# Optimization experiments

Measured on AMD Instinct MI355X. Metric: run time of the kernel, lower is better.

The kernel has to match this reference:

```python
import jax, jax.numpy as jnp
import numpy as np

N_NODES = 50000
N_EDGES = 800000
F_IN = 2
T = 12
HID = 64
OUT = 12
K = 2  # diffusion order: identity + 1-hop (out- and in-directed)


def setup_inputs() -> dict:
    key = jax.random.key(0)
    ks = jax.random.split(key, 12)
    inp = {}
    inp["x"] = jax.random.normal(ks[0], (1, N_NODES, F_IN, T), dtype=jnp.float32)
    inp["edge_index"] = jax.random.randint(ks[1], (2, N_EDGES), 0, N_NODES)
    inp["edge_weight"] = jax.random.uniform(ks[2], (N_EDGES,), dtype=jnp.float32)

    def u(k, shape, fan):
        s = 1.0 / np.sqrt(fan)
        return jax.random.uniform(k, shape, jnp.float32, -s, s)

    c1 = F_IN + HID   # 66: DCRNN gates operate on cat([X, H])
    c2 = HID + HID    # 128
    inp["w1z"] = u(ks[3], (2, K, c1, HID), c1); inp["b1z"] = jnp.zeros((HID,), jnp.float32)
    inp["w1r"] = u(ks[4], (2, K, c1, HID), c1); inp["b1r"] = jnp.zeros((HID,), jnp.float32)
    inp["w1h"] = u(ks[5], (2, K, c1, HID), c1); inp["b1h"] = jnp.zeros((HID,), jnp.float32)
    inp["w2z"] = u(ks[6], (2, K, c2, HID), c2); inp["b2z"] = jnp.zeros((HID,), jnp.float32)
    inp["w2r"] = u(ks[7], (2, K, c2, HID), c2); inp["b2r"] = jnp.zeros((HID,), jnp.float32)
    inp["w2h"] = u(ks[8], (2, K, c2, HID), c2); inp["b2h"] = jnp.zeros((HID,), jnp.float32)
    inp["lin_w"] = u(ks[9], (HID, OUT), HID)
    inp["lin_b"] = u(ks[10], (OUT,), HID)
    return inp


def _dconv(X, row, col, norm_out, norm_in, w, b):
    # K=2 diffusion conv: H = X@W[:,0] + (D_O^-1 W diffusion)@W[0,1] + (D_I^-1 W^T diffusion)@W[1,1] + b
    H = X @ w[0, 0] + X @ w[1, 0]
    Xr = X[row]  # gather source-node features per edge: [E, C]
    Tx_o = jax.ops.segment_sum(norm_out[:, None] * Xr, col, num_segments=N_NODES)
    Tx_i = jax.ops.segment_sum(norm_in[:, None] * Xr, col, num_segments=N_NODES)
    return H + Tx_o @ w[0, 1] + Tx_i @ w[1, 1] + b


def _cell(X, H, row, col, no, ni, wz, bz, wr, br, wh, bh):
    # GRU-style DCRNN cell
    XH = jnp.concatenate([X, H], axis=1)
    Z = jax.nn.sigmoid(_dconv(XH, row, col, no, ni, wz, bz))
    R = jax.nn.sigmoid(_dconv(XH, row, col, no, ni, wr, br))
    Ht = jnp.tanh(_dconv(jnp.concatenate([X, R * H], axis=1), row, col, no, ni, wh, bh))
    return Z * H + (1.0 - Z) * Ht


def reference(x, edge_index, edge_weight, w1z, b1z, w1r, b1r, w1h, b1h,
              w2z, b2z, w2r, b2r, w2h, b2h, lin_w, lin_b):
    row, col = edge_index[0], edge_index[1]
    deg_out = jax.ops.segment_sum(edge_weight, row, num_segments=N_NODES)
    deg_in = jax.ops.segment_sum(edge_weight, col, num_segments=N_NODES)
    norm_out = edge_weight / deg_out[row]  # per-edge weight of D_O^{-1} W
    norm_in = edge_weight / deg_in[col]    # per-edge weight of D_I^{-1} W^T
    xs = jnp.transpose(x[0], (2, 0, 1))    # [T, N, F] (batch = 1)

    def step(carry, xt):
        h1, h2 = carry
        h1 = jax.nn.relu(_cell(xt, h1, row, col, norm_out, norm_in, w1z, b1z, w1r, b1r, w1h, b1h))
        h2 = jax.nn.relu(_cell(h1, h2, row, col, norm_out, norm_in, w2z, b2z, w2r, b2r, w2h, b2h))
        return (h1, h2), None

    h0 = jnp.zeros((N_NODES, HID), x.dtype)
    (h1, h2), _ = jax.lax.scan(step, (h0, h0), xs)
    out = h2 @ lin_w + lin_b  # [N, 12]
    return out.reshape(1, N_NODES, OUT)
```

## Files before the change

### kernel.cpp

```cpp
#include <hip/hip_runtime.h>

#define NN 50000
#define NE 800000
#define TT 12
#define NBIN (4 * NN)
#define NBLK ((NBIN + 255) / 256)

typedef _Float16 h16;
typedef __attribute__((ext_vector_type(2))) _Float16 h16x2;
typedef __attribute__((ext_vector_type(4))) _Float16 h16x4;
typedef __attribute__((ext_vector_type(8))) _Float16 half8;
typedef __attribute__((ext_vector_type(4))) float f32x4;
typedef __attribute__((address_space(3))) h16 as3h16;
typedef __attribute__((address_space(3))) half8 as3half8;

static constexpr size_t alignup(size_t x) { return (x + 255) & ~(size_t)255; }
static constexpr size_t O_CNT  = 0;
static constexpr size_t O_CUR  = alignup(O_CNT + NBIN + 1);
static constexpr size_t O_DEGO = alignup(O_CUR + NBIN);
static constexpr size_t O_BSUM = alignup(O_DEGO + NN);
static constexpr size_t O_BEXC = O_BSUM + 1024;
static constexpr size_t O_EDG  = alignup(O_BEXC + 1024);
static constexpr size_t O_TXX  = alignup(O_EDG + (size_t)NE * 2);
static constexpr size_t O_WF1ZR= alignup(O_TXX + (size_t)TT * NN * 4);
static constexpr size_t O_WF1H = alignup(O_WF1ZR + 12288);
static constexpr size_t O_WF2ZR= alignup(O_WF1H + 6144);
static constexpr size_t O_WF2H = alignup(O_WF2ZR + 24576);
static constexpr size_t O_WX1ZR= alignup(O_WF2H + 12288);
static constexpr size_t O_WX1H = alignup(O_WX1ZR + 768);
static constexpr size_t O_PX0  = alignup(O_WX1H + 384);
static constexpr size_t O_PX1  = O_PX0 + (size_t)NN * 64;
static constexpr size_t O_PZR  = O_PX1 + (size_t)NN * 64;
static constexpr size_t O_Z1   = O_PZR + (size_t)NN * 64;
static constexpr size_t O_Z2   = O_Z1 + (size_t)NN * 32;
static constexpr size_t O_TXA  = alignup(O_Z2 + (size_t)NN * 32);
static constexpr size_t O_TXB  = alignup(O_TXA + (size_t)NN * 64);
static constexpr size_t WS_FLOATS = O_TXB + (size_t)NN * 128;

__device__ __forceinline__ float sigm_(float x) { return 1.f / (1.f + __expf(-x)); }
__device__ __forceinline__ float tanh_(float x) { float e = __expf(2.f * x); return 1.f - 2.f / (e + 1.f); }

__device__ __forceinline__ void gld_lds16(const h16* g, as3h16* l) {
    __builtin_amdgcn_global_load_lds(
        (const __attribute__((address_space(1))) void*)g,
        (__attribute__((address_space(3))) void*)l, 16, 0, 0);
}


__global__ __launch_bounds__(256) void k_zero(float* ws) {
    size_t i = (size_t)blockIdx.x * 256 + threadIdx.x;
    size_t stride = (size_t)gridDim.x * 256;
    for (size_t p = i; p < O_BSUM + 2048; p += stride) ((int*)ws)[p] = 0;
    for (size_t p = i; p < (size_t)NN * 128; p += stride) ws[O_PX0 + p] = 0.f;
    for (size_t p = i; p < (size_t)NN * 128; p += stride) ws[O_TXB + p] = 0.f;
}

__global__ __launch_bounds__(256) void k_hist(const int* ei, float* ws) {
    int e = blockIdx.x * 256 + threadIdx.x;
    if (e >= NE) return;
    int r = ei[e], c = ei[NE + e];
    int bin = c * 4 + r / 12500;
    int rk = atomicAdd((int*)ws + O_CNT + bin, 1);
    ((int*)ws)[O_TXX + e] = rk;
}

__global__ __launch_bounds__(256) void k_scanA(float* ws) {
    __shared__ int sh[256];
    int t = threadIdx.x, i = blockIdx.x * 256 + t;
    int v = (i < NBIN) ? ((int*)ws)[O_CNT + i] : 0;
    sh[t] = v; __syncthreads();
    for (int o = 128; o > 0; o >>= 1) { if (t < o) sh[t] += sh[t + o]; __syncthreads(); }
    if (t == 0) ((int*)ws)[O_BSUM + blockIdx.x] = sh[0];
}

__global__ __launch_bounds__(256) void k_scanB(float* ws) {
    __shared__ int tot[256];
    int t = threadIdx.x;
    int* bsum = (int*)ws + O_BSUM;
    int* bexc = (int*)ws + O_BEXC;
    int base = t * 4;
    int v0 = (base + 0 < NBLK) ? bsum[base + 0] : 0;
    int v1 = (base + 1 < NBLK) ? bsum[base + 1] : 0;
    int v2 = (base + 2 < NBLK) ? bsum[base + 2] : 0;
    int v3 = (base + 3 < NBLK) ? bsum[base + 3] : 0;
    int sum = v0 + v1 + v2 + v3;
    tot[t] = sum; __syncthreads();
    for (int o = 1; o < 256; o <<= 1) {
        int a = (t >= o) ? tot[t - o] : 0;
        __syncthreads(); tot[t] += a; __syncthreads();
    }
    int excl = tot[t] - sum;
    if (base + 0 < NBLK) bexc[base + 0] = excl;
    if (base + 1 < NBLK) bexc[base + 1] = excl + v0;
    if (base + 2 < NBLK) bexc[base + 2] = excl + v0 + v1;
    if (base + 3 < NBLK) bexc[base + 3] = excl + v0 + v1 + v2;
    if (t == 255) ((int*)ws)[O_CNT + NBIN] = tot[255];
}

__global__ __launch_bounds__(256) void k_scanC(float* ws) {
    __shared__ int sh[256];
    int t = threadIdx.x, b = blockIdx.x, i = b * 256 + t;
    int v = (i < NBIN) ? ((int*)ws)[O_CNT + i] : 0;
    sh[t] = v; __syncthreads();
    for (int o = 1; o < 256; o <<= 1) {
        int a = (t >= o) ? sh[t - o] : 0;
        __syncthreads(); sh[t] += a; __syncthreads();
    }
    if (i < NBIN) ((int*)ws)[O_CNT + i] = ((int*)ws)[O_BEXC + b] + sh[t] - v;
}

__global__ __launch_bounds__(256) void k_scatter(const int* ei, const float* ew, float* ws) {
    int e = blockIdx.x * 256 + threadIdx.x;
    if (e >= NE) return;
    int r = ei[e], c = ei[NE + e];
    float w = ew[e];
    atomicAdd(ws + O_DEGO + r, w);
    int bin = c * 4 + r / 12500;
    int p = ((const int*)ws)[O_CNT + bin] + ((const int*)ws)[O_TXX + e];
    uint2 rec; rec.x = (unsigned)r; rec.y = __float_as_uint(w);
    ((uint2*)(ws + O_EDG))[p] = rec;
}

__global__ __launch_bounds__(256) void k_norm(float* ws) {
    int n = blockIdx.x * 4 + (threadIdx.x >> 6);
    int lane = threadIdx.x & 63;
    const int* offs = (const int*)ws + O_CNT;
    uint2* recs = (uint2*)(ws + O_EDG);
    const float* dego = ws + O_DEGO;
    int e0 = offs[4 * n], e1 = offs[4 * n + 4];
    float s = 0.f;
    for (int e = e0 + lane; e < e1; e += 64) s += __uint_as_float(recs[e].y);
    #pragma unroll
    for (int m = 1; m < 64; m <<= 1) s += __shfl_xor(s, m);
    float inv = 1.f / s;
    for (int e = e0 + lane; e < e1; e += 64) {
        uint2 r = recs[e];
        float w = __uint_as_float(r.y);
        h16x2 nv; nv.x = (h16)(w / dego[r.x]); nv.y = (h16)(w * inv);
        r.y = __builtin_bit_cast(unsigned int, nv);
        recs[e] = r;
    }
}

__global__ __launch_bounds__(256) void k_aggx(const float* __restrict__ x, float* __restrict__ ws) {
    int tid = threadIdx.x;
    int n = blockIdx.x * 8 + (tid >> 5);
    int l = tid & 31;
    const int* offs = (const int*)ws + O_CNT;
    const uint2* recs = (const uint2*)(ws + O_EDG);
    int e0 = offs[4 * n], e1 = offs[4 * n + 4];
    int f = l / 12, tt2 = l % 12;
    bool act = l < 24;
    float ao = 0.f, ai = 0.f;
    uint2 rc0, rc1;
    if (e0 < e1) {
        rc0 = recs[e0];
        rc1 = recs[(e0 + 1 < e1) ? e0 + 1 : e1 - 1];
    }
    for (int e = e0; e < e1; e += 2) {
        uint2 c0 = rc0, c1 = rc1;
        int n2 = (e + 2 < e1) ? e + 2 : e1 - 1, n3 = (e + 3 < e1) ? e + 3 : e1 - 1;
        rc0 = recs[n2]; rc1 = recs[n3];
        h16x2 nv0 = __builtin_bit_cast(h16x2, c0.y);
        h16x2 nv1 = __builtin_bit_cast(h16x2, c1.y);
        bool ok1 = (e + 1 < e1);
        float no1 = ok1 ? (float)nv1.x : 0.f, ni1 = ok1 ? (float)nv1.y : 0.f;
        if (act) {
            float v0 = x[(size_t)c0.x * 24 + f * 12 + tt2];
            float v1 = x[(size_t)c1.x * 24 + f * 12 + tt2];
            ao += (float)nv0.x * v0 + no1 * v1;
            ai += (float)nv0.y * v0 + ni1 * v1;
        }
    }
    if (act) {
        ws[O_TXX + ((size_t)tt2 * NN + n) * 4 + f] = ao;
        ws[O_TXX + ((size_t)tt2 * NN + n) * 4 + 2 + f] = ai;
    }
}

__device__ void packf_dev(int L, int NO, const float* wa, const float* wb, h16* Wf, int idx) {
    int C = (L == 1) ? 66 : 128;
    int NT = NO / 16;
    int j = idx & 7, l = (idx >> 3) & 63;
    int rest = idx >> 9;
    int ct = rest % NT, ks = rest / NT;
    int k = ks * 32 + ((l >> 4) << 3) + j;
    int col = ct * 16 + (l & 15);
    const float* w = wa; int jj = col;
    if (NO == 128 && col >= 64) { w = wb; jj = col - 64; }
    int G = k >> 6, c6 = k & 63, sg, crow;
    if (L == 1) { sg = G; crow = 2 + c6; }
    else        { sg = G >> 1; crow = ((G & 1) << 6) + c6; }
    float v;
    if (sg == 0)      v = w[(size_t)(0 * C + crow) * 64 + jj] + w[(size_t)(2 * C + crow) * 64 + jj];
    else if (sg == 1) v = w[(size_t)(1 * C + crow) * 64 + jj];
    else              v = w[(size_t)(3 * C + crow) * 64 + jj];
    Wf[idx] = (h16)v;
}

__device__ void packx_dev(int NO, const float* wa, const float* wb, float* Wx, int idx) {
    if (idx >= 6 * NO) return;
    int cc = idx / NO, col = idx % NO;
    const float* w = wa; int jj = col;
    if (NO == 128 && col >= 64) { w = wb; jj = col - 64; }
    int sg = cc >> 1, c = cc & 1;
    float v;
    if (sg == 0)      v = w[(size_t)(0 * 66 + c) * 64 + jj] + w[(size_t)(2 * 66 + c) * 64 + jj];
    else if (sg == 1) v = w[(size_t)(1 * 66 + c) * 64 + jj];
    else              v = w[(size_t)(3 * 66 + c) * 64 + jj];
    Wx[idx] = v;
}

__global__ __launch_bounds__(256) void k_packall(const float* w1z, const float* w1r, const float* w1h,
    const float* w2z, const float* w2r, const float* w2h, float* ws) {
    int b = blockIdx.x, t = threadIdx.x;
    if (b < 96)       packf_dev(1, 128, w1z, w1r, (h16*)(ws + O_WF1ZR), b * 256 + t);
    else if (b < 144) packf_dev(1, 64,  w1h, nullptr, (h16*)(ws + O_WF1H), (b - 96) * 256 + t);
    else if (b < 336) packf_dev(2, 128, w2z, w2r, (h16*)(ws + O_WF2ZR), (b - 144) * 256 + t);
    else if (b < 432) packf_dev(2, 64,  w2h, nullptr, (h16*)(ws + O_WF2H), (b - 336) * 256 + t);
    else {
        int idx = (b - 432) * 256 + t;
        if (idx < 768) packx_dev(128, w1z, w1r, ws + O_WX1ZR, idx);
        int idx2 = idx - 768;
        if (idx2 >= 0 && idx2 < 384) packx_dev(64, w1h, nullptr, ws + O_WX1H, idx2);
    }
}

__global__ __launch_bounds__(256) void k_aggP(
    const h16* __restrict__ T,
    h16* __restrict__ outA, int orsA, int oA, int iA,
    h16* __restrict__ outB, int orsB, int oB, int iB,
    const float* __restrict__ ws) {
    int tid = threadIdx.x, lane = tid & 63, wv = tid >> 6;
    int q = lane >> 4, fl = lane & 15;
    int n = blockIdx.x * 16 + wv * 4 + q;
    const int* offs = (const int*)ws + O_CNT;
    const uint2* recs = (const uint2*)(ws + O_EDG);
    int e0 = offs[4 * n], e1 = offs[4 * n + 4];
    float ao[8] = {}, ai[8] = {};
    for (int e = e0; e < e1; e += 4) {
        int i1 = e + 1 < e1 ? e + 1 : e1 - 1;
        int i2 = e + 2 < e1 ? e + 2 : e1 - 1;
        int i3 = e + 3 < e1 ? e + 3 : e1 - 1;
        uint2 r0 = recs[e], r1 = recs[i1], r2 = recs[i2], r3 = recs[i3];
        half8 v0 = *(const half8*)(T + (size_t)r0.x * 128 + fl * 8);
        half8 v1 = *(const half8*)(T + (size_t)r1.x * 128 + fl * 8);
        half8 v2 = *(const half8*)(T + (size_t)r2.x * 128 + fl * 8);
        half8 v3 = *(const half8*)(T + (size_t)r3.x * 128 + fl * 8);
        h16x2 m0 = __builtin_bit_cast(h16x2, r0.y);
        h16x2 m1 = __builtin_bit_cast(h16x2, r1.y);
        h16x2 m2 = __builtin_bit_cast(h16x2, r2.y);
        h16x2 m3 = __builtin_bit_cast(h16x2, r3.y);
        float no0 = (float)m0.x, ni0 = (float)m0.y;
        float no1 = (e + 1 < e1) ? (float)m1.x : 0.f, ni1 = (e + 1 < e1) ? (float)m1.y : 0.f;
        float no2 = (e + 2 < e1) ? (float)m2.x : 0.f, ni2 = (e + 2 < e1) ? (float)m2.y : 0.f;
        float no3 = (e + 3 < e1) ? (float)m3.x : 0.f, ni3 = (e + 3 < e1) ? (float)m3.y : 0.f;
        #pragma unroll
        for (int j = 0; j < 8; ++j) {
            float f0 = (float)v0[j], f1 = (float)v1[j], f2 = (float)v2[j], f3 = (float)v3[j];
            ao[j] += no0 * f0 + no1 * f1 + no2 * f2 + no3 * f3;
            ai[j] += ni0 * f0 + ni1 * f1 + ni2 * f2 + ni3 * f3;
        }
    }
    h16* outP = (fl < 8) ? outA : outB;
    int ors = (fl < 8) ? orsA : orsB;
    int fo = (fl < 8) ? fl : fl - 8;
    int oT = ((fl < 8) ? oA : oB) + fo * 8;
    int iT = ((fl < 8) ? iA : iB) + fo * 8;
    half8 wo, wi;
    #pragma unroll
    for (int j = 0; j < 8; ++j) { wo[j] = (h16)ao[j]; wi[j] = (h16)ai[j]; }
    *(half8*)(outP + (size_t)n * ors + oT) = wo;
    *(half8*)(outP + (size_t)n * ors + iT) = wi;
}

__global__ __launch_bounds__(256) void k_agg1(
    const h16* __restrict__ T, int hs,
    h16* __restrict__ out, int ors, int oA, int iA,
    const float* __restrict__ ws) {
    int tid = threadIdx.x, lane = tid & 63, wv = tid >> 6;
    int q = lane >> 3, fl = lane & 7;
    int n = blockIdx.x * 32 + wv * 8 + q;
    if (n >= NN) n = NN - 1;
    const int* offs = (const int*)ws + O_CNT;
    const uint2* recs = (const uint2*)(ws + O_EDG);
    int e0 = offs[4 * n], e1 = offs[4 * n + 4];
    float ao[8] = {}, ai[8] = {};
    for (int e = e0; e < e1; e += 2) {
        int i1 = e + 1 < e1 ? e + 1 : e1 - 1;
        uint2 r0 = recs[e], r1 = recs[i1];
        half8 v0 = *(const half8*)(T + (size_t)r0.x * hs + fl * 8);
        half8 v1 = *(const half8*)(T + (size_t)r1.x * hs + fl * 8);
        h16x2 m0 = __builtin_bit_cast(h16x2, r0.y);
        h16x2 m1 = __builtin_bit_cast(h16x2, r1.y);
        float no0 = (float)m0.x, ni0 = (float)m0.y;
        float no1 = (e + 1 < e1) ? (float)m1.x : 0.f, ni1 = (e + 1 < e1) ? (float)m1.y : 0.f;
        #pragma unroll
        for (int j = 0; j < 8; ++j) {
            float f0 = (float)v0[j], f1 = (float)v1[j];
            ao[j] += no0 * f0 + no1 * f1;
            ai[j] += ni0 * f0 + ni1 * f1;
        }
    }
    half8 wo, wi;
    #pragma unroll
    for (int j = 0; j < 8; ++j) { wo[j] = (h16)ao[j]; wi[j] = (h16)ai[j]; }
    *(half8*)(out + (size_t)n * ors + oA + fl * 8) = wo;
    *(half8*)(out + (size_t)n * ors + iA + fl * 8) = wi;
}

struct Seg { const h16* p[6]; int st[6]; int of[6]; };
#define RB ((NN + 63) / 64)

template <int NG, int NO, int CT, int EPI, int XEPI>
__device__ __forceinline__ void mmg_body(int bi, const Seg& seg, const h16* __restrict__ Wf,
    const float* __restrict__ Wx, const float* __restrict__ x, const float* __restrict__ txx, int t,
    const float* __restrict__ Ba, const float* __restrict__ Bb,
    const h16* Hprev, h16* zbuf, h16* rhh, h16* houth, as3h16* lds) {
    constexpr int KS = NG * 2;
    constexpr int NT = NO / 16;
    int tid = threadIdx.x, lane = tid & 63, wv = tid >> 6;
    int ctb = (wv & 1) * CT;
    int brow = bi * 64;
    int row0 = brow + (wv >> 1) * 32;
    int r16 = lane & 15, kg = lane >> 4;

    {
        int gr0 = brow + wv * 16 + r16; if (gr0 >= NN) gr0 = NN - 1;
        #pragma unroll
        for (int G = 0; G < NG; ++G) {
            const h16* bpg = seg.p[G] + (size_t)gr0 * seg.st[G] + seg.of[G] + kg * 8;
            #pragma unroll
            for (int sub = 0; sub < 2; ++sub)
                gld_lds16(bpg + sub * 32, lds + (size_t)(G * 8 + sub * 4 + wv) * 512);
        }
    }
    __syncthreads();

    f32x4 acc[2][CT];
    #pragma unroll
    for (int s = 0; s < 2; ++s)
        #pragma unroll
        for (int c = 0; c < CT; ++c) acc[s][c] = (f32x4){0.f, 0.f, 0.f, 0.f};

    #pragma unroll
    for (int ks = 0; ks < KS; ++ks) {
        int G = ks >> 1;
        half8 af[2], bf[CT];
        #pragma unroll
        for (int s = 0; s < 2; ++s) {
            int ib = G * 8 + (ks & 1) * 4 + (wv >> 1) * 2 + s;
            af[s] = *(const as3half8*)(lds + (size_t)ib * 512 + lane * 8);
        }
        #pragma unroll
        for (int c = 0; c < CT; ++c)
            bf[c] = *(const half8*)(Wf + (((size_t)ks * NT + ctb + c) * 64 + lane) * 8);
        #pragma unroll
        for (int c = 0; c < CT; ++c)
            #pragma unroll
            for (int s = 0; s < 2; ++s)
                acc[s][c] = __builtin_amdgcn_mfma_f32_16x16x32_f16(af[s], bf[c], acc[s][c], 0, 0, 0);
    }

    int rg4 = (lane >> 4) * 4;
    #pragma unroll
    for (int s = 0; s < 2; ++s) {
        int rbase = row0 + s * 16 + rg4;
        float xa0[4], xa1[4]; float4 tg[4];
        if (XEPI) {
            #pragma unroll
            for (int r = 0; r < 4; ++r) {
                int row = rbase + r; if (row >= NN) row = NN - 1;
                xa0[r] = x[(size_t)row * 24 + t];
                xa1[r] = x[(size_t)row * 24 + 12 + t];
                tg[r] = *(const float4*)&txx[((size_t)t * NN + row) * 4];
            }
        }
        #pragma unroll
        for (int c = 0; c < CT; ++c) {
            int col = (ctb + c) * 16 + r16;
            float w0, w1, w2, w3, w4, w5;
            if (XEPI) {
                w0 = Wx[col]; w1 = Wx[NO + col]; w2 = Wx[2 * NO + col];
                w3 = Wx[3 * NO + col]; w4 = Wx[4 * NO + col]; w5 = Wx[5 * NO + col];
            }
            float bb = (EPI == 0) ? (col < 64 ? Ba[col] : Bb[col - 64]) : Ba[col];
            #pragma unroll
            for (int r = 0; r < 4; ++r) {
                int row = rbase + r;
                if (row >= NN) continue;
                float v = acc[s][c][r] + bb;
                if (XEPI) v += xa0[r] * w0 + xa1[r] * w1 + tg[r].x * w2 + tg[r].y * w3 + tg[r].z * w4 + tg[r].w * w5;
                if (EPI == 0) {
                    if (col < 64) zbuf[(size_t)row * 64 + col] = (h16)sigm_(v);
                    else {
                        float rr_ = sigm_(v);
                        float hp = (float)Hprev[(size_t)row * 128 + col - 64];
                        rhh[(size_t)row * 128 + col - 64] = (h16)(rr_ * hp);
                    }
                } else {
                    float ht = tanh_(v);
                    float z = (float)zbuf[(size_t)row * 64 + col];
                    float hp = (float)Hprev[(size_t)row * 128 + col];
                    float hn = fmaxf(z * hp + (1.f - z) * ht, 0.f);
                    houth[(size_t)row * 128 + col] = (h16)hn;
                }
            }
        }
    }
}

template <int NG, int NO, int CT, int EPI, int XEPI>
__global__ __launch_bounds__(256) void k_mmg(Seg seg, const h16* __restrict__ Wf,
    const float* __restrict__ Wx, const float* __restrict__ x, const float* __restrict__ txx, int t,
    const float* __restrict__ Ba, const float* __restrict__ Bb,
    const h16* Hprev, h16* zbuf, h16* rhh, h16* houth) {
    __shared__ __align__(16) h16 smem[NG * 4096];
    mmg_body<NG, NO, CT, EPI, XEPI>(blockIdx.x, seg, Wf, Wx, x, txx, t, Ba, Bb, Hprev, zbuf, rhh, houth,
                                    (as3h16*)smem);
}

__global__ __launch_bounds__(256) void k_mmzr2(Seg sA, Seg sB,
    const h16* __restrict__ wfA, const h16* __restrict__ wfB, const float* __restrict__ wxB,
    const float* __restrict__ x, const float* __restrict__ txx, int tB,
    const float* __restrict__ bAz, const float* __restrict__ bAr,
    const float* __restrict__ bBz, const float* __restrict__ bBr,
    const h16* hpA, h16* zA, h16* rhA,
    const h16* hpB, h16* zB, h16* rhB) {
    __shared__ __align__(16) h16 smem[6 * 4096];
    if (blockIdx.x < RB)
        mmg_body<6, 128, 4, 0, 0>(blockIdx.x, sA, wfA, nullptr, nullptr, nullptr, 0, bAz, bAr,
                                  hpA, zA, rhA, nullptr, (as3h16*)smem);
    else
        mmg_body<3, 128, 4, 0, 1>(blockIdx.x - RB, sB, wfB, wxB, x, txx, tB, bBz, bBr,
                                  hpB, zB, rhB, nullptr, (as3h16*)smem);
}

__global__ __launch_bounds__(256) void k_mmh2(Seg sA, Seg sB,
    const h16* __restrict__ wfA, const h16* __restrict__ wfB, const float* __restrict__ wxB,
    const float* __restrict__ x, const float* __restrict__ txx, int tB,
    const float* __restrict__ bAh, const float* __restrict__ bBh,
    h16* zA, const h16* hpA, h16* hoA,
    h16* zB, const h16* hpB, h16* hoB) {
    __shared__ __align__(16) h16 smem[6 * 4096];
    if (blockIdx.x < RB)
        mmg_body<6, 64, 2, 1, 0>(blockIdx.x, sA, wfA, nullptr, nullptr, nullptr, 0, bAh, nullptr,
                                 hpA, zA, nullptr, hoA, (as3h16*)smem);
    else
        mmg_body<3, 64, 2, 1, 1>(blockIdx.x - RB, sB, wfB, wxB, x, txx, tB, bBh, nullptr,
                                 hpB, zB, nullptr, hoB, (as3h16*)smem);
}

__global__ __launch_bounds__(256) void k_final(const h16* __restrict__ h2p, const float* __restrict__ lw,
                                               const float* __restrict__ lb, float* __restrict__ out) {
    __shared__ float sh[16 * 65];
    int t = threadIdx.x;
    int n0 = blockIdx.x * 16;
    int idx = t * 4;
    int nl = idx >> 6, h = idx & 63;
    h16x4 v = *(const h16x4*)&h2p[(size_t)(n0 + nl) * 128 + h];
    sh[nl * 65 + h] = (float)v[0]; sh[nl * 65 + h + 1] = (float)v[1];
    sh[nl * 65 + h + 2] = (float)v[2]; sh[nl * 65 + h + 3] = (float)v[3];
    __syncthreads();
    if (t < 192) {
        int n = t / 12, o = t % 12;
        float acc = lb[o];
        #pragma unroll 8
        for (int k = 0; k < 64; ++k) acc += sh[n * 65 + k] * lw[k * 12 + o];
        out[(size_t)(n0 + n) * 12 + o] = acc;
    }
}

extern "C" void kernel_launch(void* const* d_in, const int* in_sizes, int n_in,
                              void* d_out, int out_size, void* d_ws, size_t ws_size,
                              hipStream_t stream) {
    const float* x   = (const float*)d_in[0];
    const int*   ei  = (const int*)d_in[1];
    const float* ew  = (const float*)d_in[2];
    const float* w1z = (const float*)d_in[3];  const float* b1z = (const float*)d_in[4];
    const float* w1r = (const float*)d_in[5];  const float* b1r = (const float*)d_in[6];
    const float* w1h = (const float*)d_in[7];  const float* b1h = (const float*)d_in[8];
    const float* w2z = (const float*)d_in[9];  const float* b2z = (const float*)d_in[10];
    const float* w2r = (const float*)d_in[11]; const float* b2r = (const float*)d_in[12];
    const float* w2h = (const float*)d_in[13]; const float* b2h = (const float*)d_in[14];
    const float* lw  = (const float*)d_in[15]; const float* lb  = (const float*)d_in[16];
    float* out = (float*)d_out;
    float* ws  = (float*)d_ws;
    if (ws_size < WS_FLOATS * sizeof(float)) return;

    k_zero<<<2048, 256, 0, stream>>>(ws);
    k_hist<<<(NE + 255) / 256, 256, 0, stream>>>(ei, ws);
    k_scanA<<<NBLK, 256, 0, stream>>>(ws);
    k_scanB<<<1, 256, 0, stream>>>(ws);
    k_scanC<<<NBLK, 256, 0, stream>>>(ws);
    k_scatter<<<(NE + 255) / 256, 256, 0, stream>>>(ei, ew, ws);
    k_norm<<<NN / 4, 256, 0, stream>>>(ws);
    k_aggx<<<NN / 8, 256, 0, stream>>>(x, ws);
    k_packall<<<437, 256, 0, stream>>>(w1z, w1r, w1h, w2z, w2r, w2h, ws);

    h16* pEven = (h16*)(ws + O_PX0);
    h16* pOdd  = (h16*)(ws + O_PX1);
    h16* pzr   = (h16*)(ws + O_PZR);
    h16* z1    = (h16*)(ws + O_Z1);
    h16* z2    = (h16*)(ws + O_Z2);
    h16* txA = (h16*)(ws + O_TXA);
    h16* txB = (h16*)(ws + O_TXB);
    const float* txx = ws + O_TXX;
    const h16* wf1zr = (const h16*)(ws + O_WF1ZR);
    const h16* wf1h  = (const h16*)(ws + O_WF1H);
    const h16* wf2zr = (const h16*)(ws + O_WF2ZR);
    const h16* wf2h  = (const h16*)(ws + O_WF2H);
    const float* wx1zr = ws + O_WX1ZR;
    const float* wx1h  = ws + O_WX1H;
    const int GAP = NN / 16;
    const int GA1 = (NN + 31) / 32;

    auto s1zr = [&](h16* px) -> Seg {
        return {{px, txB, txB, nullptr, nullptr, nullptr}, {128, 256, 256, 0, 0, 0}, {0, 0, 128, 0, 0, 0}};
    };
    Seg s1h = {{pzr, txA, txA, nullptr, nullptr, nullptr}, {128, 128, 128, 0, 0, 0}, {0, 0, 64, 0, 0, 0}};
    auto s2zr = [&](h16* px) -> Seg {
        return {{px, px, txB, txB, txB, txB}, {128, 128, 256, 256, 256, 256}, {0, 64, 0, 64, 128, 192}};
    };
    auto s2h = [&](h16* px) -> Seg {
        return {{px, pzr, txB, txB, txB, txB}, {128, 128, 256, 256, 256, 256}, {0, 64, 0, 64, 128, 192}};
    };

    k_mmg<3, 128, 4, 0, 1><<<RB, 256, 0, stream>>>(s1zr(pOdd), wf1zr, wx1zr, x, txx, 0,
        b1z, b1r, pOdd, z1, pzr, nullptr);
    k_agg1<<<GA1, 256, 0, stream>>>(pzr, 128, txA, 128, 0, 64, ws);
    k_mmg<3, 64, 2, 1, 1><<<RB, 256, 0, stream>>>(s1h, wf1h, wx1h, x, txx, 0,
        b1h, nullptr, pOdd, z1, nullptr, pEven);
    k_aggP<<<GAP, 256, 0, stream>>>(pEven, txB, 256, 0, 128, txB, 256, 64, 192, ws);

    for (int t = 0; t < TT - 1; ++t) {
        h16* pxT  = (t & 1) ? pOdd : pEven;
        h16* pxT1 = (t & 1) ? pEven : pOdd;
        k_mmzr2<<<RB * 2, 256, 0, stream>>>(s2zr(pxT), s1zr(pxT), wf2zr, wf1zr, wx1zr,
            x, txx, t + 1, b2z, b2r, b1z, b1r,
            pxT + 64, z2, pzr + 64,
            pxT,      z1, pzr);
        k_aggP<<<GAP, 256, 0, stream>>>(pzr, txA, 128, 0, 64, txB, 256, 64, 192, ws);
        k_mmh2<<<RB * 2, 256, 0, stream>>>(s2h(pxT), s1h, wf2h, wf1h, wx1h,
            x, txx, t + 1, b2h, b1h,
            z2, pxT + 64, pxT1 + 64,
            z1, pxT,      pxT1);
        k_aggP<<<GAP, 256, 0, stream>>>(pxT1, txB, 256, 0, 128, txB, 256, 64, 192, ws);
    }

    k_mmg<6, 128, 4, 0, 0><<<RB, 256, 0, stream>>>(s2zr(pOdd), wf2zr, nullptr, nullptr, nullptr, 0,
        b2z, b2r, pOdd + 64, z2, pzr + 64, nullptr);
    k_agg1<<<GA1, 256, 0, stream>>>(pzr + 64, 128, txB, 256, 64, 192, ws);
    k_mmg<6, 64, 2, 1, 0><<<RB, 256, 0, stream>>>(s2h(pOdd), wf2h, nullptr, nullptr, nullptr, 0,
        b2h, nullptr, pOdd + 64, z2, nullptr, pEven + 64);
    k_final<<<NN / 16, 256, 0, stream>>>(pEven + 64, lw, lb, out);
}
```

Before: 1.818 ms.

## Make gate GEMM kernels persistent with register-resident weights and double-buffered LDS

The gate GEMM kernels now launch a fixed grid of 256 blocks per segment that loop over row tiles instead of one block per 64-row tile. Weight fragments are loaded into registers once per block rather than reloaded every k-step. The next tile's activations are staged into a second LDS buffer while the current tile computes. This targets repeated weight loads and exposed global-to-LDS latency, at the cost of much higher register pressure (up to 48 half8 weight registers in the 6-group case), doubled LDS, and occupancy of only one block per CU.

After: 2.214 ms. 21.8% more time.

```diff
diff --git a/kernel.cpp b/kernel.cpp
--- a/kernel.cpp
+++ b/kernel.cpp
@@ -313,142 +313,153 @@
 #define RB ((NN + 63) / 64)
 
 template <int NG, int NO, int CT, int EPI, int XEPI>
-__device__ __forceinline__ void mmg_body(int bi, const Seg& seg, const h16* __restrict__ Wf,
+__device__ __forceinline__ void pers_body(int pb, int nb, const Seg& seg, const h16* __restrict__ Wf,
     const float* __restrict__ Wx, const float* __restrict__ x, const float* __restrict__ txx, int t,
     const float* __restrict__ Ba, const float* __restrict__ Bb,
     const h16* Hprev, h16* zbuf, h16* rhh, h16* houth, as3h16* lds) {
     constexpr int KS = NG * 2;
     constexpr int NT = NO / 16;
+    constexpr int BUFH = NG * 4096;
     int tid = threadIdx.x, lane = tid & 63, wv = tid >> 6;
     int ctb = (wv & 1) * CT;
-    int brow = bi * 64;
-    int row0 = brow + (wv >> 1) * 32;
     int r16 = lane & 15, kg = lane >> 4;
-
-    {
-        int gr0 = brow + wv * 16 + r16; if (gr0 >= NN) gr0 = NN - 1;
+    int rg4 = (lane >> 4) * 4;
+
+    half8 wreg[KS][CT];
+    #pragma unroll
+    for (int ks = 0; ks < KS; ++ks)
+        #pragma unroll
+        for (int c = 0; c < CT; ++c)
+            wreg[ks][c] = *(const half8*)(Wf + (((size_t)ks * NT + ctb + c) * 64 + lane) * 8);
+
+    auto stage = [&](int bi, int b) {
+        int gr0 = bi * 64 + wv * 16 + r16; if (gr0 >= NN) gr0 = NN - 1;
         #pragma unroll
         for (int G = 0; G < NG; ++G) {
             const h16* bpg = seg.p[G] + (size_t)gr0 * seg.st[G] + seg.of[G] + kg * 8;
             #pragma unroll
             for (int sub = 0; sub < 2; ++sub)
-                gld_lds16(bpg + sub * 32, lds + (size_t)(G * 8 + sub * 4 + wv) * 512);
+                gld_lds16(bpg + sub * 32, lds + (size_t)b * BUFH + (size_t)(G * 8 + sub * 4 + wv) * 512);
         }
-    }
-    __syncthreads();
-
-    f32x4 acc[2][CT];
-    #pragma unroll
-    for (int s = 0; s < 2; ++s)
-        #pragma unroll
-        for (int c = 0; c < CT; ++c) acc[s][c] = (f32x4){0.f, 0.f, 0.f, 0.f};
-
-    #pragma unroll
-    for (int ks = 0; ks < KS; ++ks) {
-        int G = ks >> 1;
-        half8 af[2], bf[CT];
+    };
+
+    int buf = 0;
+    stage(pb, 0);
+    for (int bi = pb; bi < RB; bi += nb) {
+        __syncthreads();
+        if (bi + nb < RB) stage(bi + nb, buf ^ 1);
+
+        int row0 = bi * 64 + (wv >> 1) * 32;
+        f32x4 acc[2][CT];
+        #pragma unroll
+        for (int s = 0; s < 2; ++s)
+            #pragma unroll
+            for (int c = 0; c < CT; ++c) acc[s][c] = (f32x4){0.f, 0.f, 0.f, 0.f};
+
+        #pragma unroll
+        for (int ks = 0; ks < KS; ++ks) {
+            int G = ks >> 1;
+            half8 af[2];
+            #pragma unroll
+            for (int s = 0; s < 2; ++s) {
+                int ib = G * 8 + (ks & 1) * 4 + (wv >> 1) * 2 + s;
+                af[s] = *(const as3half8*)(lds + (size_t)buf * BUFH + (size_t)ib * 512 + lane * 8);
+            }
+            #pragma unroll
+            for (int c = 0; c < CT; ++c)
+                #pragma unroll
+                for (int s = 0; s < 2; ++s)
+                    acc[s][c] = __builtin_amdgcn_mfma_f32_16x16x32_f16(af[s], wreg[ks][c], acc[s][c], 0, 0, 0);
+        }
+
         #pragma unroll
         for (int s = 0; s < 2; ++s) {
-            int ib = G * 8 + (ks & 1) * 4 + (wv >> 1) * 2 + s;
-            af[s] = *(const as3half8*)(lds + (size_t)ib * 512 + lane * 8);
-        }
-        #pragma unroll
-        for (int c = 0; c < CT; ++c)
-            bf[c] = *(const half8*)(Wf + (((size_t)ks * NT + ctb + c) * 64 + lane) * 8);
-        #pragma unroll
-        for (int c = 0; c < CT; ++c)
+            int rbase = row0 + s * 16 + rg4;
+            float xa0[4], xa1[4]; float4 tg[4];
+            if (XEPI) {
+                #pragma unroll
+                for (int r = 0; r < 4; ++r) {
+                    int row = rbase + r; if (row >= NN) row = NN - 1;
+                    xa0[r] = x[(size_t)row * 24 + t];
+                    xa1[r] = x[(size_t)row * 24 + 12 + t];
+                    tg[r] = *(const float4*)&txx[((size_t)t * NN + row) * 4];
+                }
+            }
             #pragma unroll
-            for (int s = 0; s < 2; ++s)
-                acc[s][c] = __builtin_amdgcn_mfma_f32_16x16x32_f16(af[s], bf[c], acc[s][c], 0, 0, 0);
-    }
-
-    int rg4 = (lane >> 4) * 4;
-    #pragma unroll
-    for (int s = 0; s < 2; ++s) {
-        int rbase = row0 + s * 16 + rg4;
-        float xa0[4], xa1[4]; float4 tg[4];
-        if (XEPI) {
-            #pragma unroll
-            for (int r = 0; r < 4; ++r) {
-                int row = rbase + r; if (row >= NN) row = NN - 1;
-                xa0[r] = x[(size_t)row * 24 + t];
-                xa1[r] = x[(size_t)row * 24 + 12 + t];
-                tg[r] = *(const float4*)&txx[((size_t)t * NN + row) * 4];
-            }
-        }
-        #pragma unroll
-        for (int c = 0; c < CT; ++c) {
-            int col = (ctb + c) * 16 + r16;
-            float w0, w1, w2, w3, w4, w5;
-            if (XEPI) {
-                w0 = Wx[col]; w1 = Wx[NO + col]; w2 = Wx[2 * NO + col];
-                w3 = Wx[3 * NO + col]; w4 = Wx[4 * NO + col]; w5 = Wx[5 * NO + col];
-            }
-            float bb = (EPI == 0) ? (col < 64 ? Ba[col] : Bb[col - 64]) : Ba[col];
-            #pragma unroll
-            for (int r = 0; r < 4; ++r) {
-                int row = rbase + r;
-                if (row >= NN) continue;
-                float v = acc[s][c][r] + bb;
-                if (XEPI) v += xa0[r] * w0 + xa1[r] * w1 + tg[r].x * w2 + tg[r].y * w3 + tg[r].z * w4 + tg[r].w * w5;
-                if (EPI == 0) {
-                    if (col < 64) zbuf[(size_t)row * 64 + col] = (h16)sigm_(v);
-                    else {
-                        float rr_ = sigm_(v);
-                        float hp = (float)Hprev[(size_t)row * 128 + col - 64];
-                        rhh[(size_t)row * 128 + col - 64] = (h16)(rr_ * hp);
+            for (int c = 0; c < CT; ++c) {
+                int col = (ctb + c) * 16 + r16;
+                float w0, w1, w2, w3, w4, w5;
+                if (XEPI) {
+                    w0 = Wx[col]; w1 = Wx[NO + col]; w2 = Wx[2 * NO + col];
+                    w3 = Wx[3 * NO + col]; w4 = Wx[4 * NO + col]; w5 = Wx[5 * NO + col];
+                }
+                float bb = (EPI == 0) ? (col < 64 ? Ba[col] : Bb[col - 64]) : Ba[col];
+                #pragma unroll
+                for (int r = 0; r < 4; ++r) {
+                    int row = rbase + r;
+                    if (row >= NN) continue;
+                    float v = acc[s][c][r] + bb;
+                    if (XEPI) v += xa0[r] * w0 + xa1[r] * w1 + tg[r].x * w2 + tg[r].y * w3 + tg[r].z * w4 + tg[r].w * w5;
+                    if (EPI == 0) {
+                        if (col < 64) zbuf[(size_t)row * 64 + col] = (h16)sigm_(v);
+                        else {
+                            float rr_ = sigm_(v);
+                            float hp = (float)Hprev[(size_t)row * 128 + col - 64];
+                            rhh[(size_t)row * 128 + col - 64] = (h16)(rr_ * hp);
+                        }
+                    } else {
+                        float ht = tanh_(v);
+                        float z = (float)zbuf[(size_t)row * 64 + col];
+                        float hp = (float)Hprev[(size_t)row * 128 + col];
+                        float hn = fmaxf(z * hp + (1.f - z) * ht, 0.f);
+                        houth[(size_t)row * 128 + col] = (h16)hn;
                     }
-                } else {
-                    float ht = tanh_(v);
-                    float z = (float)zbuf[(size_t)row * 64 + col];
-                    float hp = (float)Hprev[(size_t)row * 128 + col];
-                    float hn = fmaxf(z * hp + (1.f - z) * ht, 0.f);
-                    houth[(size_t)row * 128 + col] = (h16)hn;
                 }
             }
         }
+        buf ^= 1;
     }
 }
 
 template <int NG, int NO, int CT, int EPI, int XEPI>
-__global__ __launch_bounds__(256) void k_mmg(Seg seg, const h16* __restrict__ Wf,
+__global__ __launch_bounds__(256, 1) void k_pmm(Seg seg, const h16* __restrict__ Wf,
     const float* __restrict__ Wx, const float* __restrict__ x, const float* __restrict__ txx, int t,
     const float* __restrict__ Ba, const float* __restrict__ Bb,
     const h16* Hprev, h16* zbuf, h16* rhh, h16* houth) {
-    __shared__ __align__(16) h16 smem[NG * 4096];
-    mmg_body<NG, NO, CT, EPI, XEPI>(blockIdx.x, seg, Wf, Wx, x, txx, t, Ba, Bb, Hprev, zbuf, rhh, houth,
-                                    (as3h16*)smem);
-}
-
-__global__ __launch_bounds__(256) void k_mmzr2(Seg sA, Seg sB,
+    __shared__ __align__(16) h16 smem[2 * NG * 4096];
+    pers_body<NG, NO, CT, EPI, XEPI>(blockIdx.x, 256, seg, Wf, Wx, x, txx, t, Ba, Bb,
+                                     Hprev, zbuf, rhh, houth, (as3h16*)smem);
+}
+
+__global__ __launch_bounds__(256, 1) void k_pzr2(Seg sA, Seg sB,
     const h16* __restrict__ wfA, const h16* __restrict__ wfB, const float* __restrict__ wxB,
     const float* __restrict__ x, const float* __restrict__ txx, int tB,
     const float* __restrict__ bAz, const float* __restrict__ bAr,
     const float* __restrict__ bBz, const float* __restrict__ bBr,
     const h16* hpA, h16* zA, h16* rhA,
     const h16* hpB, h16* zB, h16* rhB) {
-    __shared__ __align__(16) h16 smem[6 * 4096];
-    if (blockIdx.x < RB)
-        mmg_body<6, 128, 4, 0, 0>(blockIdx.x, sA, wfA, nullptr, nullptr, nullptr, 0, bAz, bAr,
-                                  hpA, zA, rhA, nullptr, (as3h16*)smem);
+    __shared__ __align__(16) h16 smem[2 * 6 * 4096];
+    if (blockIdx.x < 256)
+        pers_body<6, 128, 4, 0, 0>(blockIdx.x, 256, sA, wfA, nullptr, nullptr, nullptr, 0, bAz, bAr,
+                                   hpA, zA, rhA, nullptr, (as3h16*)smem);
     else
-        mmg_body<3, 128, 4, 0, 1>(blockIdx.x - RB, sB, wfB, wxB, x, txx, tB, bBz, bBr,
-                                  hpB, zB, rhB, nullptr, (as3h16*)smem);
-}
-
-__global__ __launch_bounds__(256) void k_mmh2(Seg sA, Seg sB,
+        pers_body<3, 128, 4, 0, 1>(blockIdx.x - 256, 256, sB, wfB, wxB, x, txx, tB, bBz, bBr,
+                                   hpB, zB, rhB, nullptr, (as3h16*)smem);
+}
+
+__global__ __launch_bounds__(256, 1) void k_ph2(Seg sA, Seg sB,
     const h16* __restrict__ wfA, const h16* __restrict__ wfB, const float* __restrict__ wxB,
     const float* __restrict__ x, const float* __restrict__ txx, int tB,
     const float* __restrict__ bAh, const float* __restrict__ bBh,
     h16* zA, const h16* hpA, h16* hoA,
     h16* zB, const h16* hpB, h16* hoB) {
-    __shared__ __align__(16) h16 smem[6 * 4096];
-    if (blockIdx.x < RB)
-        mmg_body<6, 64, 2, 1, 0>(blockIdx.x, sA, wfA, nullptr, nullptr, nullptr, 0, bAh, nullptr,
-                                 hpA, zA, nullptr, hoA, (as3h16*)smem);
+    __shared__ __align__(16) h16 smem[2 * 6 * 4096];
+    if (blockIdx.x < 256)
+        pers_body<6, 64, 2, 1, 0>(blockIdx.x, 256, sA, wfA, nullptr, nullptr, nullptr, 0, bAh, nullptr,
+                                  hpA, zA, nullptr, hoA, (as3h16*)smem);
     else
-        mmg_body<3, 64, 2, 1, 1>(blockIdx.x - RB, sB, wfB, wxB, x, txx, tB, bBh, nullptr,
-                                 hpB, zB, nullptr, hoB, (as3h16*)smem);
+        pers_body<3, 64, 2, 1, 1>(blockIdx.x - 256, 256, sB, wfB, wxB, x, txx, tB, bBh, nullptr,
+                                  hpB, zB, nullptr, hoB, (as3h16*)smem);
 }
 
 __global__ __launch_bounds__(256) void k_final(const h16* __restrict__ h2p, const float* __restrict__ lw,
@@ -526,32 +537,32 @@
         return {{px, pzr, txB, txB, txB, txB}, {128, 128, 256, 256, 256, 256}, {0, 64, 0, 64, 128, 192}};
     };
 
-    k_mmg<3, 128, 4, 0, 1><<<RB, 256, 0, stream>>>(s1zr(pOdd), wf1zr, wx1zr, x, txx, 0,
+    k_pmm<3, 128, 4, 0, 1><<<256, 256, 0, stream>>>(s1zr(pOdd), wf1zr, wx1zr, x, txx, 0,
         b1z, b1r, pOdd, z1, pzr, nullptr);
     k_agg1<<<GA1, 256, 0, stream>>>(pzr, 128, txA, 128, 0, 64, ws);
-    k_mmg<3, 64, 2, 1, 1><<<RB, 256, 0, stream>>>(s1h, wf1h, wx1h, x, txx, 0,
+    k_pmm<3, 64, 2, 1, 1><<<256, 256, 0, stream>>>(s1h, wf1h, wx1h, x, txx, 0,
         b1h, nullptr, pOdd, z1, nullptr, pEven);
     k_aggP<<<GAP, 256, 0, stream>>>(pEven, txB, 256, 0, 128, txB, 256, 64, 192, ws);
 
     for (int t = 0; t < TT - 1; ++t) {
         h16* pxT  = (t & 1) ? pOdd : pEven;
         h16* pxT1 = (t & 1) ? pEven : pOdd;
-        k_mmzr2<<<RB * 2, 256, 0, stream>>>(s2zr(pxT), s1zr(pxT), wf2zr, wf1zr, wx1zr,
+        k_pzr2<<<512, 256, 0, stream>>>(s2zr(pxT), s1zr(pxT), wf2zr, wf1zr, wx1zr,
             x, txx, t + 1, b2z, b2r, b1z, b1r,
             pxT + 64, z2, pzr + 64,
             pxT,      z1, pzr);
         k_aggP<<<GAP, 256, 0, stream>>>(pzr, txA, 128, 0, 64, txB, 256, 64, 192, ws);
-        k_mmh2<<<RB * 2, 256, 0, stream>>>(s2h(pxT), s1h, wf2h, wf1h, wx1h,
+        k_ph2<<<512, 256, 0, stream>>>(s2h(pxT), s1h, wf2h, wf1h, wx1h,
             x, txx, t + 1, b2h, b1h,
             z2, pxT + 64, pxT1 + 64,
             z1, pxT,      pxT1);
         k_aggP<<<GAP, 256, 0, stream>>>(pxT1, txB, 256, 0, 128, txB, 256, 64, 192, ws);
     }
 
-    k_mmg<6, 128, 4, 0, 0><<<RB, 256, 0, stream>>>(s2zr(pOdd), wf2zr, nullptr, nullptr, nullptr, 0,
+    k_pmm<6, 128, 4, 0, 0><<<256, 256, 0, stream>>>(s2zr(pOdd), wf2zr, nullptr, nullptr, nullptr, 0,
         b2z, b2r, pOdd + 64, z2, pzr + 64, nullptr);
     k_agg1<<<GA1, 256, 0, stream>>>(pzr + 64, 128, txB, 256, 64, 192, ws);
-    k_mmg<6, 64, 2, 1, 0><<<RB, 256, 0, stream>>>(s2h(pOdd), wf2h, nullptr, nullptr, nullptr, 0,
+    k_pmm<6, 64, 2, 1, 0><<<256, 256, 0, stream>>>(s2h(pOdd), wf2h, nullptr, nullptr, nullptr, 0,
         b2h, nullptr, pOdd + 64, z2, nullptr, pEven + 64);
     k_final<<<NN / 16, 256, 0, stream>>>(pEven + 64, lw, lb, out);
 }
```

## Pipeline gather-matmul K-slices through a 4-slot LDS ring with 512-thread blocks

Applied to the files above, without the earlier changes.

The fused gather-GEMM body moves to 512 threads (8 waves split into 4 column quarters and 2 row halves). Each wave preloads its weight fragments into registers once. Activation K-groups stream into a 4-slot LDS ring via global_load_lds with explicit vmcnt waits, so MFMA work on one group overlaps the loads of the next. This replaces the old scheme of staging every group up front, cutting LDS per block to allow more resident blocks, at the cost of more barriers and higher register pressure from the weight preload.

New measurement: 1.695 ms. -6.8%, faster.

```diff
diff --git a/kernel.cpp b/kernel.cpp
--- a/kernel.cpp
+++ b/kernel.cpp
@@ -44,6 +44,13 @@
     __builtin_amdgcn_global_load_lds(
         (const __attribute__((address_space(1))) void*)g,
         (__attribute__((address_space(3))) void*)l, 16, 0, 0);
+}
+
+template <int N>
+__device__ __forceinline__ void wait_lgkm0_vm() {
+    if constexpr (N == 0)      asm volatile("s_waitcnt lgkmcnt(0) vmcnt(0)" ::: "memory");
+    else if constexpr (N == 1) asm volatile("s_waitcnt lgkmcnt(0) vmcnt(1)" ::: "memory");
+    else                       asm volatile("s_waitcnt lgkmcnt(0) vmcnt(2)" ::: "memory");
 }
 
 
@@ -312,6 +319,39 @@
 struct Seg { const h16* p[6]; int st[6]; int of[6]; };
 #define RB ((NN + 63) / 64)
 
+template <int G>
+__device__ __forceinline__ void stage_g(as3h16* lds, const Seg& seg, int bi, int lane, int rh, int cq) {
+    int r16 = lane & 15, kg = lane >> 4;
+    int gr0 = bi * 64 + cq * 16 + r16; if (gr0 >= NN) gr0 = NN - 1;
+    gld_lds16(seg.p[G] + (size_t)gr0 * seg.st[G] + seg.of[G] + rh * 32 + kg * 8,
+              lds + (G & 3) * 4096 + (rh * 4 + cq) * 512);
+}
+
+template <int G, int NG, int CT>
+__device__ __forceinline__ void gsteps(as3h16* lds, const Seg& seg, int bi, int lane, int rh, int cq,
+                                       half8 (&wreg)[NG * 2][CT], f32x4 (&acc)[2][CT]) {
+    if constexpr (G < NG) {
+        constexpr int OUT = (NG - 1 - G) >= 2 ? 2 : (NG - 1 - G);
+        wait_lgkm0_vm<OUT>();
+        __builtin_amdgcn_s_barrier();
+        asm volatile("" ::: "memory");
+        if constexpr (G + 3 < NG) stage_g<G + 3>(lds, seg, bi, lane, rh, cq);
+        #pragma unroll
+        for (int kk = 0; kk < 2; ++kk) {
+            half8 af[2];
+            #pragma unroll
+            for (int s = 0; s < 2; ++s)
+                af[s] = *(const as3half8*)(lds + (G & 3) * 4096 + (kk * 4 + rh * 2 + s) * 512 + lane * 8);
+            #pragma unroll
+            for (int c = 0; c < CT; ++c)
+                #pragma unroll
+                for (int s = 0; s < 2; ++s)
+                    acc[s][c] = __builtin_amdgcn_mfma_f32_16x16x32_f16(af[s], wreg[2 * G + kk][c], acc[s][c], 0, 0, 0);
+        }
+        gsteps<G + 1, NG, CT>(lds, seg, bi, lane, rh, cq, wreg, acc);
+    }
+}
+
 template <int NG, int NO, int CT, int EPI, int XEPI>
 __device__ __forceinline__ void mmg_body(int bi, const Seg& seg, const h16* __restrict__ Wf,
     const float* __restrict__ Wx, const float* __restrict__ x, const float* __restrict__ txx, int t,
@@ -320,22 +360,20 @@
     constexpr int KS = NG * 2;
     constexpr int NT = NO / 16;
     int tid = threadIdx.x, lane = tid & 63, wv = tid >> 6;
-    int ctb = (wv & 1) * CT;
-    int brow = bi * 64;
-    int row0 = brow + (wv >> 1) * 32;
-    int r16 = lane & 15, kg = lane >> 4;
-
-    {
-        int gr0 = brow + wv * 16 + r16; if (gr0 >= NN) gr0 = NN - 1;
+    int cq = wv & 3, rh = wv >> 2;
+    int ctb = cq * CT;
+    int r16 = lane & 15;
+
+    half8 wreg[KS][CT];
+    #pragma unroll
+    for (int ks = 0; ks < KS; ++ks)
         #pragma unroll
-        for (int G = 0; G < NG; ++G) {
-            const h16* bpg = seg.p[G] + (size_t)gr0 * seg.st[G] + seg.of[G] + kg * 8;
-            #pragma unroll
-            for (int sub = 0; sub < 2; ++sub)
-                gld_lds16(bpg + sub * 32, lds + (size_t)(G * 8 + sub * 4 + wv) * 512);
-        }
-    }
-    __syncthreads();
+        for (int c = 0; c < CT; ++c)
+            wreg[ks][c] = *(const half8*)(Wf + (((size_t)ks * NT + ctb + c) * 64 + lane) * 8);
+
+    stage_g<0>(lds, seg, bi, lane, rh, cq);
+    stage_g<1>(lds, seg, bi, lane, rh, cq);
+    stage_g<2>(lds, seg, bi, lane, rh, cq);
 
     f32x4 acc[2][CT];
     #pragma unroll
@@ -343,25 +381,9 @@
         #pragma unroll
         for (int c = 0; c < CT; ++c) acc[s][c] = (f32x4){0.f, 0.f, 0.f, 0.f};
 
-    #pragma unroll
-    for (int ks = 0; ks < KS; ++ks) {
-        int G = ks >> 1;
-        half8 af[2], bf[CT];
-        #pragma unroll
-        for (int s = 0; s < 2; ++s) {
-            int ib = G * 8 + (ks & 1) * 4 + (wv >> 1) * 2 + s;
-            af[s] = *(const as3half8*)(lds + (size_t)ib * 512 + lane * 8);
-        }
-        #pragma unroll
-        for (int c = 0; c < CT; ++c)
-            bf[c] = *(const half8*)(Wf + (((size_t)ks * NT + ctb + c) * 64 + lane) * 8);
-        #pragma unroll
-        for (int c = 0; c < CT; ++c)
-            #pragma unroll
-            for (int s = 0; s < 2; ++s)
-                acc[s][c] = __builtin_amdgcn_mfma_f32_16x16x32_f16(af[s], bf[c], acc[s][c], 0, 0, 0);
-    }
-
+    gsteps<0, NG, CT>(lds, seg, bi, lane, rh, cq, wreg, acc);
+
+    int row0 = bi * 64 + rh * 32;
     int rg4 = (lane >> 4) * 4;
     #pragma unroll
     for (int s = 0; s < 2; ++s) {
@@ -411,43 +433,43 @@
 }
 
 template <int NG, int NO, int CT, int EPI, int XEPI>
-__global__ __launch_bounds__(256) void k_mmg(Seg seg, const h16* __restrict__ Wf,
+__global__ __launch_bounds__(512, 2) void k_mmg(Seg seg, const h16* __restrict__ Wf,
     const float* __restrict__ Wx, const float* __restrict__ x, const float* __restrict__ txx, int t,
     const float* __restrict__ Ba, const float* __restrict__ Bb,
     const h16* Hprev, h16* zbuf, h16* rhh, h16* houth) {
-    __shared__ __align__(16) h16 smem[NG * 4096];
+    __shared__ __align__(16) h16 smem[4 * 4096];
     mmg_body<NG, NO, CT, EPI, XEPI>(blockIdx.x, seg, Wf, Wx, x, txx, t, Ba, Bb, Hprev, zbuf, rhh, houth,
                                     (as3h16*)smem);
 }
 
-__global__ __launch_bounds__(256) void k_mmzr2(Seg sA, Seg sB,
+__global__ __launch_bounds__(512, 2) void k_mmzr2(Seg sA, Seg sB,
     const h16* __restrict__ wfA, const h16* __restrict__ wfB, const float* __restrict__ wxB,
     const float* __restrict__ x, const float* __restrict__ txx, int tB,
     const float* __restrict__ bAz, const float* __restrict__ bAr,
     const float* __restrict__ bBz, const float* __restrict__ bBr,
     const h16* hpA, h16* zA, h16* rhA,
     const h16* hpB, h16* zB, h16* rhB) {
-    __shared__ __align__(16) h16 smem[6 * 4096];
+    __shared__ __align__(16) h16 smem[4 * 4096];
     if (blockIdx.x < RB)
-        mmg_body<6, 128, 4, 0, 0>(blockIdx.x, sA, wfA, nullptr, nullptr, nullptr, 0, bAz, bAr,
+        mmg_body<6, 128, 2, 0, 0>(blockIdx.x, sA, wfA, nullptr, nullptr, nullptr, 0, bAz, bAr,
                                   hpA, zA, rhA, nullptr, (as3h16*)smem);
     else
-        mmg_body<3, 128, 4, 0, 1>(blockIdx.x - RB, sB, wfB, wxB, x, txx, tB, bBz, bBr,
+        mmg_body<3, 128, 2, 0, 1>(blockIdx.x - RB, sB, wfB, wxB, x, txx, tB, bBz, bBr,
                                   hpB, zB, rhB, nullptr, (as3h16*)smem);
 }
 
-__global__ __launch_bounds__(256) void k_mmh2(Seg sA, Seg sB,
+__global__ __launch_bounds__(512, 2) void k_mmh2(Seg sA, Seg sB,
     const h16* __restrict__ wfA, const h16* __restrict__ wfB, const float* __restrict__ wxB,
     const float* __restrict__ x, const float* __restrict__ txx, int tB,
     const float* __restrict__ bAh, const float* __restrict__ bBh,
     h16* zA, const h16* hpA, h16* hoA,
     h16* zB, const h16* hpB, h16* hoB) {
-    __shared__ __align__(16) h16 smem[6 * 4096];
+    __shared__ __align__(16) h16 smem[4 * 4096];
     if (blockIdx.x < RB)
-        mmg_body<6, 64, 2, 1, 0>(blockIdx.x, sA, wfA, nullptr, nullptr, nullptr, 0, bAh, nullptr,
+        mmg_body<6, 64, 1, 1, 0>(blockIdx.x, sA, wfA, nullptr, nullptr, nullptr, 0, bAh, nullptr,
                                  hpA, zA, nullptr, hoA, (as3h16*)smem);
     else
-        mmg_body<3, 64, 2, 1, 1>(blockIdx.x - RB, sB, wfB, wxB, x, txx, tB, bBh, nullptr,
+        mmg_body<3, 64, 1, 1, 1>(blockIdx.x - RB, sB, wfB, wxB, x, txx, tB, bBh, nullptr,
                                  hpB, zB, nullptr, hoB, (as3h16*)smem);
 }
 
@@ -526,32 +548,32 @@
         return {{px, pzr, txB, txB, txB, txB}, {128, 128, 256, 256, 256, 256}, {0, 64, 0, 64, 128, 192}};
     };
 
-    k_mmg<3, 128, 4, 0, 1><<<RB, 256, 0, stream>>>(s1zr(pOdd), wf1zr, wx1zr, x, txx, 0,
+    k_mmg<3, 128, 2, 0, 1><<<RB, 512, 0, stream>>>(s1zr(pOdd), wf1zr, wx1zr, x, txx, 0,
         b1z, b1r, pOdd, z1, pzr, nullptr);
     k_agg1<<<GA1, 256, 0, stream>>>(pzr, 128, txA, 128, 0, 64, ws);
-    k_mmg<3, 64, 2, 1, 1><<<RB, 256, 0, stream>>>(s1h, wf1h, wx1h, x, txx, 0,
+    k_mmg<3, 64, 1, 1, 1><<<RB, 512, 0, stream>>>(s1h, wf1h, wx1h, x, txx, 0,
         b1h, nullptr, pOdd, z1, nullptr, pEven);
     k_aggP<<<GAP, 256, 0, stream>>>(pEven, txB, 256, 0, 128, txB, 256, 64, 192, ws);
 
     for (int t = 0; t < TT - 1; ++t) {
         h16* pxT  = (t & 1) ? pOdd : pEven;
         h16* pxT1 = (t & 1) ? pEven : pOdd;
-        k_mmzr2<<<RB * 2, 256, 0, stream>>>(s2zr(pxT), s1zr(pxT), wf2zr, wf1zr, wx1zr,
+        k_mmzr2<<<RB * 2, 512, 0, stream>>>(s2zr(pxT), s1zr(pxT), wf2zr, wf1zr, wx1zr,
             x, txx, t + 1, b2z, b2r, b1z, b1r,
             pxT + 64, z2, pzr + 64,
             pxT,      z1, pzr);
         k_aggP<<<GAP, 256, 0, stream>>>(pzr, txA, 128, 0, 64, txB, 256, 64, 192, ws);
-        k_mmh2<<<RB * 2, 256, 0, stream>>>(s2h(pxT), s1h, wf2h, wf1h, wx1h,
+        k_mmh2<<<RB * 2, 512, 0, stream>>>(s2h(pxT), s1h, wf2h, wf1h, wx1h,
             x, txx, t + 1, b2h, b1h,
             z2, pxT + 64, pxT1 + 64,
             z1, pxT,      pxT1);
         k_aggP<<<GAP, 256, 0, stream>>>(pxT1, txB, 256, 0, 128, txB, 256, 64, 192, ws);
     }
 
-    k_mmg<6, 128, 4, 0, 0><<<RB, 256, 0, stream>>>(s2zr(pOdd), wf2zr, nullptr, nullptr, nullptr, 0,
+    k_mmg<6, 128, 2, 0, 0><<<RB, 512, 0, stream>>>(s2zr(pOdd), wf2zr, nullptr, nullptr, nullptr, 0,
         b2z, b2r, pOdd + 64, z2, pzr + 64, nullptr);
     k_agg1<<<GA1, 256, 0, stream>>>(pzr + 64, 128, txB, 256, 64, 192, ws);
-    k_mmg<6, 64, 2, 1, 0><<<RB, 256, 0, stream>>>(s2h(pOdd), wf2h, nullptr, nullptr, nullptr, 0,
+    k_mmg<6, 64, 1, 1, 0><<<RB, 512, 0, stream>>>(s2h(pOdd), wf2h, nullptr, nullptr, nullptr, 0,
         b2h, nullptr, pOdd + 64, z2, nullptr, pEven + 64);
     k_final<<<NN / 16, 256, 0, stream>>>(pEven + 64, lw, lb, out);
 }
```
